# Performance work log

Hardware: AMD Instinct MI355X
Metric: run time of the kernel (lower is better)

Reference implementation:

```python
import jax, jax.numpy as jnp
import numpy as np

DIM = 1024
NUM_HEADS = 16
HEAD_DIM = DIM // NUM_HEADS
SCALE = HEAD_DIM ** -0.5


def setup_inputs() -> dict:
    key = jax.random.key(0)
    k1, k2, k3 = jax.random.split(key, 3)
    B, S = 2, 2048
    x = jax.random.normal(k1, (B, S, DIM), dtype=jnp.float32)
    # nn.Linear(dim, 3*dim, bias=False): store as [in, out] for x @ W
    w_qkv = jax.random.normal(k2, (DIM, 3 * DIM), dtype=jnp.float32) * (DIM ** -0.5)
    w_out = jax.random.normal(k3, (DIM, DIM), dtype=jnp.float32) * (DIM ** -0.5)
    return {"x": x, "w_qkv": w_qkv, "w_out": w_out}


def reference(x, w_qkv, w_out):
    B, S, _ = x.shape
    qkv = x @ w_qkv                               # [B,S,3*D]
    q, k, v = jnp.split(qkv, 3, axis=-1)          # each [B,S,D]
    def heads(t):
        return t.reshape(B, S, NUM_HEADS, HEAD_DIM).transpose(0, 2, 1, 3)  # [B,H,S,d]
    q, k, v = heads(q), heads(k), heads(v)
    scores = jnp.einsum('bhqd,bhkd->bhqk', q, k) * SCALE   # [B,H,S,S]
    probs = jax.nn.softmax(scores, axis=-1)
    out = jnp.einsum('bhqk,bhkd->bhqd', probs, v)          # [B,H,S,d]
    out = out.transpose(0, 2, 1, 3).reshape(B, S, DIM)
    return out @ w_out
```

## Files before the change

### kernel.cpp

```cpp
#include <hip/hip_runtime.h>


typedef __bf16 bf16x8 __attribute__((ext_vector_type(8)));
typedef __bf16 bf16x4 __attribute__((ext_vector_type(4)));
typedef float floatx4 __attribute__((ext_vector_type(4)));

#define MFMA16(a, b, c) __builtin_amdgcn_mfma_f32_16x16x32_bf16((a), (b), (c), 0, 0, 0)

#if defined(__has_builtin)
#if __has_builtin(__builtin_amdgcn_exp2f)
#define EXP2F __builtin_amdgcn_exp2f
#endif
#endif
#ifndef EXP2F
#define EXP2F exp2f
#endif

__device__ __forceinline__ unsigned pk_bf16(float a, float b) {
  union { float f; unsigned u; } ua, ub;
  ua.f = a; ub.f = b;
#if defined(__has_builtin) && __has_builtin(__builtin_amdgcn_perm)
  return __builtin_amdgcn_perm(ub.u + 0x8000u, ua.u + 0x8000u, 0x07060302u);
#else
  return ((ua.u + 0x8000u) >> 16) | ((ub.u + 0x8000u) & 0xFFFF0000u);
#endif
}

__device__ __forceinline__ void gl_lds16(const void* g, void* l) {
  __builtin_amdgcn_global_load_lds((__attribute__((address_space(1))) void*)(g),
                                   (__attribute__((address_space(3))) void*)(l),
                                   16, 0, 0);
}

__global__ __launch_bounds__(256) void prep(const float* __restrict__ x,
                                            const float* __restrict__ w_qkv,
                                            const float* __restrict__ w_out,
                                            __bf16* __restrict__ xb,
                                            __bf16* __restrict__ wqkvt,
                                            __bf16* __restrict__ woutt) {
  __shared__ float tile[64][65];
  const int bid = blockIdx.x, t = threadIdx.x;
  if (bid < 4096) {
    int i = (bid * 256 + t) * 4;
    float4 v = *(const float4*)(x + i);
    bf16x4 o = { (__bf16)v.x, (__bf16)v.y, (__bf16)v.z, (__bf16)v.w };
    *(bf16x4*)(xb + i) = o;
    return;
  }
  const float* w;
  __bf16* wt;
  int K = 1024, N, k0, n0;
  if (bid < 4864) {
    int i = bid - 4096;
    w = w_qkv; wt = wqkvt; N = 3072; k0 = (i & 15) * 64; n0 = (i >> 4) * 64;
  } else {
    int i = bid - 4864;
    w = w_out; wt = woutt; N = 1024; k0 = (i & 15) * 64; n0 = (i >> 4) * 64;
  }
  for (int j = 0; j < 16; ++j) {
    int e = j * 256 + t, r = e >> 6, c = e & 63;
    tile[r][c] = w[(size_t)(k0 + r) * N + n0 + c];
  }
  __syncthreads();
  for (int j = 0; j < 16; ++j) {
    int e = j * 256 + t, r = e >> 6, c = e & 63;
    wt[(size_t)(n0 + r) * K + k0 + c] = (__bf16)tile[c][r];
  }
}

__global__ __launch_bounds__(256) void gemm_qkv(const __bf16* __restrict__ A,
                                                const __bf16* __restrict__ Bt,
                                                __bf16* __restrict__ qkb,
                                                __bf16* __restrict__ vt) {
  constexpr int K = 1024;
  constexpr float QSCALE = 0.18033688f;
  __shared__ __align__(16) __bf16 aS[128 * 32];
  __shared__ __align__(16) __bf16 bS[128 * 32];
  const int t = threadIdx.x;
  const int lane = t & 63, wave = t >> 6;
  const int l15 = lane & 15, quad = lane >> 4;
  const int wm = wave >> 1, wn = wave & 1;
  const int m0 = blockIdx.y * 128, n0 = blockIdx.x * 128;

  const floatx4 fzero = {0.f, 0.f, 0.f, 0.f};
  floatx4 acc[4][4];
  for (int mt = 0; mt < 4; ++mt)
    for (int nt = 0; nt < 4; ++nt) acc[mt][nt] = fzero;

  const int arow = t >> 2;
  const int ach = ((t & 3) ^ (arow & 3)) * 8;
  const __bf16* gA0 = A + (size_t)(m0 + arow) * K + ach;
  const __bf16* gA1 = gA0 + (size_t)64 * K;
  const __bf16* gB0 = Bt + (size_t)(n0 + arow) * K + ach;
  const __bf16* gB1 = gB0 + (size_t)64 * K;
  const int swz = (quad ^ (l15 & 3)) * 8;

  for (int k0 = 0; k0 < K; k0 += 32) {
    __syncthreads();
    gl_lds16(gA0 + k0, (char*)aS + t * 16);
    gl_lds16(gA1 + k0, (char*)aS + 4096 + t * 16);
    gl_lds16(gB0 + k0, (char*)bS + t * 16);
    gl_lds16(gB1 + k0, (char*)bS + 4096 + t * 16);
    __syncthreads();

    bf16x8 af[4], bfr[4];
    for (int mt = 0; mt < 4; ++mt)
      af[mt] = *(const bf16x8*)(aS + (wm * 64 + mt * 16 + l15) * 32 + swz);
    for (int nt = 0; nt < 4; ++nt)
      bfr[nt] = *(const bf16x8*)(bS + (wn * 64 + nt * 16 + l15) * 32 + swz);
    for (int mt = 0; mt < 4; ++mt)
      for (int nt = 0; nt < 4; ++nt)
        acc[mt][nt] = MFMA16(af[mt], bfr[nt], acc[mt][nt]);
  }

  for (int mt = 0; mt < 4; ++mt) {
    int row = m0 + wm * 64 + mt * 16 + quad * 4;
    for (int nt = 0; nt < 4; ++nt) {
      int col0 = n0 + wn * 64 + nt * 16;
      if (col0 >= 2048) {
        int dfull = col0 + l15 - 2048;
        int bh = ((row >> 11) << 4) + (dfull >> 6);
        int d = dfull & 63, s0 = row & 2047;
        bf16x4 pk = { (__bf16)acc[mt][nt][0], (__bf16)acc[mt][nt][1],
                      (__bf16)acc[mt][nt][2], (__bf16)acc[mt][nt][3] };
        *(bf16x4*)(vt + ((size_t)bh * 64 + d) * 2048 + s0) = pk;
      } else {
        float sc = (col0 < 1024) ? QSCALE : 1.0f;
        int col = col0 + l15;
        __bf16* cp = qkb + (size_t)row * 2048 + col;
        for (int r = 0; r < 4; ++r) cp[(size_t)r * 2048] = (__bf16)(acc[mt][nt][r] * sc);
      }
    }
  }
}

__global__ __launch_bounds__(256) void gemm_n64(const __bf16* __restrict__ A,
                                                const __bf16* __restrict__ Bt,
                                                float* __restrict__ C) {
  constexpr int K = 1024, N = 1024;
  __shared__ __align__(16) __bf16 aS[128 * 32];
  __shared__ __align__(16) __bf16 bS[64 * 32];
  const int t = threadIdx.x;
  const int lane = t & 63, wave = t >> 6;
  const int l15 = lane & 15, quad = lane >> 4;
  const int m0 = blockIdx.y * 128, n0 = blockIdx.x * 64;

  const floatx4 fzero = {0.f, 0.f, 0.f, 0.f};
  floatx4 acc[2][4];
  for (int mt = 0; mt < 2; ++mt)
    for (int nt = 0; nt < 4; ++nt) acc[mt][nt] = fzero;

  const int arow = t >> 2;
  const int ach = ((t & 3) ^ (arow & 3)) * 8;
  const __bf16* gA0 = A + (size_t)(m0 + arow) * K + ach;
  const __bf16* gA1 = gA0 + (size_t)64 * K;
  const __bf16* gB0 = Bt + (size_t)(n0 + arow) * K + ach;
  const int swz = (quad ^ (l15 & 3)) * 8;

  for (int k0 = 0; k0 < K; k0 += 32) {
    __syncthreads();
    gl_lds16(gA0 + k0, (char*)aS + t * 16);
    gl_lds16(gA1 + k0, (char*)aS + 4096 + t * 16);
    gl_lds16(gB0 + k0, (char*)bS + t * 16);
    __syncthreads();

    bf16x8 af[2], bfr[4];
    for (int mt = 0; mt < 2; ++mt)
      af[mt] = *(const bf16x8*)(aS + (wave * 32 + mt * 16 + l15) * 32 + swz);
    for (int nt = 0; nt < 4; ++nt)
      bfr[nt] = *(const bf16x8*)(bS + (nt * 16 + l15) * 32 + swz);
    for (int mt = 0; mt < 2; ++mt)
      for (int nt = 0; nt < 4; ++nt)
        acc[mt][nt] = MFMA16(af[mt], bfr[nt], acc[mt][nt]);
  }

  for (int mt = 0; mt < 2; ++mt) {
    int row = m0 + wave * 32 + mt * 16 + quad * 4;
    for (int nt = 0; nt < 4; ++nt) {
      int col = n0 + nt * 16 + l15;
      float* cp = C + (size_t)row * N + col;
      for (int r = 0; r < 4; ++r) cp[(size_t)r * N] = acc[mt][nt][r];
    }
  }
}

__global__ __launch_bounds__(256) void flash_attn(const __bf16* __restrict__ qkb,
                                                  const __bf16* __restrict__ vt,
                                                  __bf16* __restrict__ out) {
  __shared__ __align__(16) __bf16 kS[2 * 64 * 64];
  __shared__ __align__(16) __bf16 vS[2 * 64 * 64];
  __shared__ __align__(16) __bf16 pT[4 * 16 * 64];

  const int t = threadIdx.x;
  const int lane = t & 63, wave = t >> 6;
  const int l15 = lane & 15, quad = lane >> 4;
  const int id = blockIdx.x;
  const int xcd = id & 7, slot = id >> 3;
  const int bh = xcd * 4 + (slot >> 4), qb = slot & 15;
  const int b = bh >> 4, h = bh & 15;

  bf16x8 qf[2][2];
  for (int qt = 0; qt < 2; ++qt) {
    const __bf16* qp = qkb +
        (size_t)(b * 2048 + qb * 128 + wave * 32 + qt * 16 + l15) * 2048 + h * 64 + quad * 8;
    qf[qt][0] = *(const bf16x8*)qp;
    qf[qt][1] = *(const bf16x8*)(qp + 32);
  }

  bf16x8 onef;
  for (int j = 0; j < 8; ++j) onef[j] = (__bf16)1.0f;

  const floatx4 fzero = {0.f, 0.f, 0.f, 0.f};
  floatx4 oacc[2][4], lacc[2];
  for (int qt = 0; qt < 2; ++qt) {
    lacc[qt] = fzero;
    for (int dt = 0; dt < 4; ++dt) oacc[qt][dt] = fzero;
  }

  const int srow = t >> 3, schk = (t & 7) ^ (srow & 7);
  const __bf16* kg0 =
      qkb + (size_t)(b * 2048 + srow) * 2048 + 1024 + h * 64 + schk * 8;
  const __bf16* kg1 = kg0 + (size_t)32 * 2048;
  const __bf16* vg0 =
      vt + (size_t)bh * 64 * 2048 + (size_t)srow * 2048 + schk * 8;
  const __bf16* vg1 = vg0 + (size_t)32 * 2048;

  const int l7 = l15 & 7;
  __bf16* pw = pT + wave * 1024 + l15 * 64;

  gl_lds16(kg0, (char*)kS + t * 16);
  gl_lds16(kg1, (char*)kS + 4096 + t * 16);
  gl_lds16(vg0, (char*)vS + t * 16);
  gl_lds16(vg1, (char*)vS + 4096 + t * 16);

  for (int nb = 0; nb < 32; ++nb) {
    __syncthreads();

    if (nb < 31) {
      const size_t n1 = (size_t)(nb + 1) * 64;
      const int oB = ((nb + 1) & 1) * 8192;
      gl_lds16(kg0 + n1 * 2048, (char*)kS + oB + t * 16);
      gl_lds16(kg1 + n1 * 2048, (char*)kS + oB + 4096 + t * 16);
      gl_lds16(vg0 + n1, (char*)vS + oB + t * 16);
      gl_lds16(vg1 + n1, (char*)vS + oB + 4096 + t * 16);
    }

    const __bf16* kC = kS + (nb & 1) * 4096;
    const __bf16* vC = vS + (nb & 1) * 4096;

    bf16x8 kf[4][2];
    for (int nt = 0; nt < 4; ++nt)
      for (int ks = 0; ks < 2; ++ks)
        kf[nt][ks] = *(const bf16x8*)(kC + (nt * 16 + l15) * 64 +
                                      ((ks * 4 + quad) ^ l7) * 8);
    bf16x8 vf[2][4];
    for (int ks = 0; ks < 2; ++ks)
      for (int dt = 0; dt < 4; ++dt)
        vf[ks][dt] = *(const bf16x8*)(vC + (dt * 16 + l15) * 64 +
                                      ((ks * 4 + quad) ^ l7) * 8);

    for (int qt = 0; qt < 2; ++qt) {
      floatx4 sa[4];
      for (int nt = 0; nt < 4; ++nt) {
        floatx4 a = fzero;
        a = MFMA16(kf[nt][0], qf[qt][0], a);
        a = MFMA16(kf[nt][1], qf[qt][1], a);
        sa[nt] = a;
      }
      for (int nt = 0; nt < 4; ++nt) {
        float p0 = EXP2F(sa[nt][0]);
        float p1 = EXP2F(sa[nt][1]);
        float p2 = EXP2F(sa[nt][2]);
        float p3 = EXP2F(sa[nt][3]);
        unsigned w0 = pk_bf16(p0, p1);
        unsigned w1 = pk_bf16(p2, p3);
        uint2 wv = {w0, w1};
        *(uint2*)((char*)pw + (((nt * 2 + (quad >> 1)) ^ l7) * 16 + (quad & 1) * 8)) = wv;
      }
      for (int ks = 0; ks < 2; ++ks) {
        bf16x8 pa = *(const bf16x8*)(pw + ((ks * 4 + quad) ^ l7) * 8);
        for (int dt = 0; dt < 4; ++dt)
          oacc[qt][dt] = MFMA16(pa, vf[ks][dt], oacc[qt][dt]);
        lacc[qt] = MFMA16(pa, onef, lacc[qt]);
      }
    }
  }

  for (int qt = 0; qt < 2; ++qt) {
    float inv[4];
    for (int r = 0; r < 4; ++r) inv[r] = 1.f / lacc[qt][r];
    __bf16* ob = out +
        (size_t)(b * 2048 + qb * 128 + wave * 32 + qt * 16 + quad * 4) * 1024 + h * 64;
    for (int dt = 0; dt < 4; ++dt)
      for (int r = 0; r < 4; ++r)
        ob[(size_t)r * 1024 + dt * 16 + l15] = (__bf16)(oacc[qt][dt][r] * inv[r]);
  }
}

extern "C" void kernel_launch(void* const* d_in, const int* in_sizes, int n_in,
                              void* d_out, int out_size, void* d_ws, size_t ws_size,
                              hipStream_t stream) {
  const float* x = (const float*)d_in[0];
  const float* w_qkv = (const float*)d_in[1];
  const float* w_out = (const float*)d_in[2];
  float* out = (float*)d_out;

  char* ws = (char*)d_ws;
  __bf16* xb = (__bf16*)(ws);
  __bf16* wqkvt = (__bf16*)(ws + ((size_t)8 << 20));
  __bf16* qkb = (__bf16*)(ws + ((size_t)16 << 20));
  __bf16* vtg = (__bf16*)(ws + ((size_t)32 << 20));
  __bf16* aout = (__bf16*)(ws + ((size_t)40 << 20));
  __bf16* woutt = (__bf16*)(ws + ((size_t)48 << 20));

  prep<<<5120, 256, 0, stream>>>(x, w_qkv, w_out, xb, wqkvt, woutt);
  gemm_qkv<<<dim3(24, 32), 256, 0, stream>>>(xb, wqkvt, qkb, vtg);
  flash_attn<<<512, 256, 0, stream>>>(qkb, vtg, aout);
  gemm_n64<<<dim3(16, 32), 256, 0, stream>>>(aout, woutt, out);
}
```

Before: 188.8 us.

## Use 8 waves per attention block with one Q tile each and MFMA priority hints

The flash attention kernel now runs 512 threads (8 waves) per block, each wave owning 16 query rows instead of 32. That halves per-wave accumulator and Q registers and lets each thread issue a single K and V async load per tile. S=QK and PV MFMA sections are wrapped in s_setprio, and the V fragment loads are moved after the softmax stage. The aim is more waves in flight to hide latency and more MFMA/exp overlap, at the cost of twice as many K/V LDS reads per query row and a larger P scratch buffer.

```diff
diff --git a/kernel.cpp b/kernel.cpp
--- a/kernel.cpp
+++ b/kernel.cpp
@@ -184,12 +184,12 @@
   }
 }
 
-__global__ __launch_bounds__(256) void flash_attn(const __bf16* __restrict__ qkb,
-                                                  const __bf16* __restrict__ vt,
-                                                  __bf16* __restrict__ out) {
+__global__ __launch_bounds__(512, 4) void flash_attn(const __bf16* __restrict__ qkb,
+                                                     const __bf16* __restrict__ vt,
+                                                     __bf16* __restrict__ out) {
   __shared__ __align__(16) __bf16 kS[2 * 64 * 64];
   __shared__ __align__(16) __bf16 vS[2 * 64 * 64];
-  __shared__ __align__(16) __bf16 pT[4 * 16 * 64];
+  __shared__ __align__(16) __bf16 pT[8 * 16 * 64];
 
   const int t = threadIdx.x;
   const int lane = t & 63, wave = t >> 6;
@@ -199,50 +199,40 @@
   const int bh = xcd * 4 + (slot >> 4), qb = slot & 15;
   const int b = bh >> 4, h = bh & 15;
 
-  bf16x8 qf[2][2];
-  for (int qt = 0; qt < 2; ++qt) {
+  bf16x8 qf[2];
+  {
     const __bf16* qp = qkb +
-        (size_t)(b * 2048 + qb * 128 + wave * 32 + qt * 16 + l15) * 2048 + h * 64 + quad * 8;
-    qf[qt][0] = *(const bf16x8*)qp;
-    qf[qt][1] = *(const bf16x8*)(qp + 32);
+        (size_t)(b * 2048 + qb * 128 + wave * 16 + l15) * 2048 + h * 64 + quad * 8;
+    qf[0] = *(const bf16x8*)qp;
+    qf[1] = *(const bf16x8*)(qp + 32);
   }
 
   bf16x8 onef;
   for (int j = 0; j < 8; ++j) onef[j] = (__bf16)1.0f;
 
   const floatx4 fzero = {0.f, 0.f, 0.f, 0.f};
-  floatx4 oacc[2][4], lacc[2];
-  for (int qt = 0; qt < 2; ++qt) {
-    lacc[qt] = fzero;
-    for (int dt = 0; dt < 4; ++dt) oacc[qt][dt] = fzero;
-  }
+  floatx4 oacc[4], lacc = fzero;
+  for (int dt = 0; dt < 4; ++dt) oacc[dt] = fzero;
 
   const int srow = t >> 3, schk = (t & 7) ^ (srow & 7);
-  const __bf16* kg0 =
+  const __bf16* kg =
       qkb + (size_t)(b * 2048 + srow) * 2048 + 1024 + h * 64 + schk * 8;
-  const __bf16* kg1 = kg0 + (size_t)32 * 2048;
-  const __bf16* vg0 =
+  const __bf16* vg =
       vt + (size_t)bh * 64 * 2048 + (size_t)srow * 2048 + schk * 8;
-  const __bf16* vg1 = vg0 + (size_t)32 * 2048;
 
   const int l7 = l15 & 7;
   __bf16* pw = pT + wave * 1024 + l15 * 64;
 
-  gl_lds16(kg0, (char*)kS + t * 16);
-  gl_lds16(kg1, (char*)kS + 4096 + t * 16);
-  gl_lds16(vg0, (char*)vS + t * 16);
-  gl_lds16(vg1, (char*)vS + 4096 + t * 16);
+  gl_lds16(kg, (char*)kS + t * 16);
+  gl_lds16(vg, (char*)vS + t * 16);
 
   for (int nb = 0; nb < 32; ++nb) {
     __syncthreads();
 
     if (nb < 31) {
-      const size_t n1 = (size_t)(nb + 1) * 64;
       const int oB = ((nb + 1) & 1) * 8192;
-      gl_lds16(kg0 + n1 * 2048, (char*)kS + oB + t * 16);
-      gl_lds16(kg1 + n1 * 2048, (char*)kS + oB + 4096 + t * 16);
-      gl_lds16(vg0 + n1, (char*)vS + oB + t * 16);
-      gl_lds16(vg1 + n1, (char*)vS + oB + 4096 + t * 16);
+      gl_lds16(kg + (size_t)(nb + 1) * 64 * 2048, (char*)kS + oB + t * 16);
+      gl_lds16(vg + (size_t)(nb + 1) * 64, (char*)vS + oB + t * 16);
     }
 
     const __bf16* kC = kS + (nb & 1) * 4096;
@@ -253,47 +243,52 @@
       for (int ks = 0; ks < 2; ++ks)
         kf[nt][ks] = *(const bf16x8*)(kC + (nt * 16 + l15) * 64 +
                                       ((ks * 4 + quad) ^ l7) * 8);
+
+    floatx4 sa[4];
+    __builtin_amdgcn_s_setprio(1);
+    for (int nt = 0; nt < 4; ++nt) {
+      floatx4 a = fzero;
+      a = MFMA16(kf[nt][0], qf[0], a);
+      a = MFMA16(kf[nt][1], qf[1], a);
+      sa[nt] = a;
+    }
+    __builtin_amdgcn_s_setprio(0);
+
+    for (int nt = 0; nt < 4; ++nt) {
+      float p0 = EXP2F(sa[nt][0]);
+      float p1 = EXP2F(sa[nt][1]);
+      float p2 = EXP2F(sa[nt][2]);
+      float p3 = EXP2F(sa[nt][3]);
+      unsigned w0 = pk_bf16(p0, p1);
+      unsigned w1 = pk_bf16(p2, p3);
+      uint2 wv = {w0, w1};
+      *(uint2*)((char*)pw + (((nt * 2 + (quad >> 1)) ^ l7) * 16 + (quad & 1) * 8)) = wv;
+    }
+
     bf16x8 vf[2][4];
     for (int ks = 0; ks < 2; ++ks)
       for (int dt = 0; dt < 4; ++dt)
         vf[ks][dt] = *(const bf16x8*)(vC + (dt * 16 + l15) * 64 +
                                       ((ks * 4 + quad) ^ l7) * 8);
 
-    for (int qt = 0; qt < 2; ++qt) {
-      floatx4 sa[4];
-      for (int nt = 0; nt < 4; ++nt) {
-        floatx4 a = fzero;
-        a = MFMA16(kf[nt][0], qf[qt][0], a);
-        a = MFMA16(kf[nt][1], qf[qt][1], a);
-        sa[nt] = a;
-      }
-      for (int nt = 0; nt < 4; ++nt) {
-        float p0 = EXP2F(sa[nt][0]);
-        float p1 = EXP2F(sa[nt][1]);
-        float p2 = EXP2F(sa[nt][2]);
-        float p3 = EXP2F(sa[nt][3]);
-        unsigned w0 = pk_bf16(p0, p1);
-        unsigned w1 = pk_bf16(p2, p3);
-        uint2 wv = {w0, w1};
-        *(uint2*)((char*)pw + (((nt * 2 + (quad >> 1)) ^ l7) * 16 + (quad & 1) * 8)) = wv;
-      }
-      for (int ks = 0; ks < 2; ++ks) {
-        bf16x8 pa = *(const bf16x8*)(pw + ((ks * 4 + quad) ^ l7) * 8);
-        for (int dt = 0; dt < 4; ++dt)
-          oacc[qt][dt] = MFMA16(pa, vf[ks][dt], oacc[qt][dt]);
-        lacc[qt] = MFMA16(pa, onef, lacc[qt]);
-      }
-    }
-  }
-
-  for (int qt = 0; qt < 2; ++qt) {
+    __builtin_amdgcn_s_setprio(1);
+    for (int ks = 0; ks < 2; ++ks) {
+      bf16x8 pa = *(const bf16x8*)(pw + ((ks * 4 + quad) ^ l7) * 8);
+      for (int dt = 0; dt < 4; ++dt)
+        oacc[dt] = MFMA16(pa, vf[ks][dt], oacc[dt]);
+      lacc = MFMA16(pa, onef, lacc);
+    }
+    __builtin_amdgcn_s_setprio(0);
+  }
+
+  {
     float inv[4];
-    for (int r = 0; r < 4; ++r) inv[r] = 1.f / lacc[qt][r];
+    for (int r = 0; r < 4; ++r) inv[r] = 1.f / lacc[r];
     __bf16* ob = out +
-        (size_t)(b * 2048 + qb * 128 + wave * 32 + qt * 16 + quad * 4) * 1024 + h * 64;
+        (size_t)(b * 2048 + qb * 128 + wave * 16 + quad * 4) * 1024 + h * 64;
     for (int dt = 0; dt < 4; ++dt)
       for (int r = 0; r < 4; ++r)
-        ob[(size_t)r * 1024 + dt * 16 + l15] = (__bf16)(oacc[qt][dt][r] * inv[r]);
+        ob[(size_t)r * 1024 + dt * 16 + l15] = (__bf16)(oacc[dt][r] * inv[r]);
   }
 }
 
@@ -315,6 +310,6 @@
 
   prep<<<5120, 256, 0, stream>>>(x, w_qkv, w_out, xb, wqkvt, woutt);
   gemm_qkv<<<dim3(24, 32), 256, 0, stream>>>(xb, wqkvt, qkb, vtg);
-  flash_attn<<<512, 256, 0, stream>>>(qkb, vtg, aout);
+  flash_attn<<<512, 512, 0, stream>>>(qkb, vtg, aout);
   gemm_n64<<<dim3(16, 32), 256, 0, stream>>>(aout, woutt, out);
 }
```

New measurement: 181.2 us. 4.0% less time.

## Keep attention probabilities in registers via permlane swaps instead of LDS round-trip

Applied to the files above, without the earlier changes.

The per-wave LDS buffer that transposed the probability tile between the QK and PV MFMAs is removed. The exp2 results are now packed with a hardware bf16 convert instruction and rearranged across lanes with permlane32/permlane16 swaps into the MFMA A-operand layout. The change also batches the QK MFMAs for both query tiles before the exponentials, adds s_setprio around the MFMA sections, and sets launch bounds to allow two blocks per CU. It removes LDS write/read traffic and the associated waits, but depends on the lane-permutation layout being correct and may raise register pressure.

```diff
diff --git a/kernel.cpp b/kernel.cpp
--- a/kernel.cpp
+++ b/kernel.cpp
@@ -17,13 +17,9 @@
 #endif
 
 __device__ __forceinline__ unsigned pk_bf16(float a, float b) {
-  union { float f; unsigned u; } ua, ub;
-  ua.f = a; ub.f = b;
-#if defined(__has_builtin) && __has_builtin(__builtin_amdgcn_perm)
-  return __builtin_amdgcn_perm(ub.u + 0x8000u, ua.u + 0x8000u, 0x07060302u);
-#else
-  return ((ua.u + 0x8000u) >> 16) | ((ub.u + 0x8000u) & 0xFFFF0000u);
-#endif
+  unsigned r;
+  asm("v_cvt_pk_bf16_f32 %0, %1, %2" : "=v"(r) : "v"(a), "v"(b));
+  return r;
 }
 
 __device__ __forceinline__ void gl_lds16(const void* g, void* l) {
@@ -184,12 +180,11 @@
   }
 }
 
-__global__ __launch_bounds__(256) void flash_attn(const __bf16* __restrict__ qkb,
-                                                  const __bf16* __restrict__ vt,
-                                                  __bf16* __restrict__ out) {
+__global__ __launch_bounds__(256, 2) void flash_attn(const __bf16* __restrict__ qkb,
+                                                     const __bf16* __restrict__ vt,
+                                                     __bf16* __restrict__ out) {
   __shared__ __align__(16) __bf16 kS[2 * 64 * 64];
   __shared__ __align__(16) __bf16 vS[2 * 64 * 64];
-  __shared__ __align__(16) __bf16 pT[4 * 16 * 64];
 
   const int t = threadIdx.x;
   const int lane = t & 63, wave = t >> 6;
@@ -226,7 +221,6 @@
   const __bf16* vg1 = vg0 + (size_t)32 * 2048;
 
   const int l7 = l15 & 7;
-  __bf16* pw = pT + wave * 1024 + l15 * 64;
 
   gl_lds16(kg0, (char*)kS + t * 16);
   gl_lds16(kg1, (char*)kS + 4096 + t * 16);
@@ -259,30 +253,44 @@
         vf[ks][dt] = *(const bf16x8*)(vC + (dt * 16 + l15) * 64 +
                                       ((ks * 4 + quad) ^ l7) * 8);
 
-    for (int qt = 0; qt < 2; ++qt) {
-      floatx4 sa[4];
+    floatx4 sa[2][4];
+    __builtin_amdgcn_s_setprio(1);
+    for (int qt = 0; qt < 2; ++qt)
       for (int nt = 0; nt < 4; ++nt) {
         floatx4 a = fzero;
         a = MFMA16(kf[nt][0], qf[qt][0], a);
         a = MFMA16(kf[nt][1], qf[qt][1], a);
-        sa[nt] = a;
+        sa[qt][nt] = a;
       }
-      for (int nt = 0; nt < 4; ++nt) {
-        float p0 = EXP2F(sa[nt][0]);
-        float p1 = EXP2F(sa[nt][1]);
-        float p2 = EXP2F(sa[nt][2]);
-        float p3 = EXP2F(sa[nt][3]);
-        unsigned w0 = pk_bf16(p0, p1);
-        unsigned w1 = pk_bf16(p2, p3);
-        uint2 wv = {w0, w1};
-        *(uint2*)((char*)pw + (((nt * 2 + (quad >> 1)) ^ l7) * 16 + (quad & 1) * 8)) = wv;
+    __builtin_amdgcn_s_setprio(0);
+
+    for (int qt = 0; qt < 2; ++qt) {
+      bf16x8 pa[2];
+      for (int ks = 0; ks < 2; ++ks) {
+        const int n0 = 2 * ks, n1 = 2 * ks + 1;
+        float e00 = EXP2F(sa[qt][n0][0]), e01 = EXP2F(sa[qt][n0][1]);
+        float e02 = EXP2F(sa[qt][n0][2]), e03 = EXP2F(sa[qt][n0][3]);
+        float e10 = EXP2F(sa[qt][n1][0]), e11 = EXP2F(sa[qt][n1][1]);
+        float e12 = EXP2F(sa[qt][n1][2]), e13 = EXP2F(sa[qt][n1][3]);
+        unsigned x0 = pk_bf16(e00, e01), x1 = pk_bf16(e02, e03);
+        unsigned y0 = pk_bf16(e10, e11), y1 = pk_bf16(e12, e13);
+        unsigned d0 = x0, d2 = y0;
+        asm("v_permlane32_swap_b32 %0, %1" : "+v"(d0), "+v"(d2));
+        asm("v_permlane16_swap_b32 %0, %1" : "+v"(d0), "+v"(d2));
+        unsigned d1 = x1, d3 = y1;
+        asm("v_permlane32_swap_b32 %0, %1" : "+v"(d1), "+v"(d3));
+        asm("v_permlane16_swap_b32 %0, %1" : "+v"(d1), "+v"(d3));
+        union { unsigned u[4]; bf16x8 v8; } pu;
+        pu.u[0] = d0; pu.u[1] = d1; pu.u[2] = d2; pu.u[3] = d3;
+        pa[ks] = pu.v8;
       }
+      __builtin_amdgcn_s_setprio(1);
       for (int ks = 0; ks < 2; ++ks) {
-        bf16x8 pa = *(const bf16x8*)(pw + ((ks * 4 + quad) ^ l7) * 8);
         for (int dt = 0; dt < 4; ++dt)
-          oacc[qt][dt] = MFMA16(pa, vf[ks][dt], oacc[qt][dt]);
-        lacc[qt] = MFMA16(pa, onef, lacc[qt]);
+          oacc[qt][dt] = MFMA16(pa[ks], vf[ks][dt], oacc[qt][dt]);
+        lacc[qt] = MFMA16(pa[ks], onef, lacc[qt]);
       }
+      __builtin_amdgcn_s_setprio(0);
     }
   }
 
```

New measurement: 173.8 us. -8.0%, faster.
